# Performance work log

Hardware: AMD Instinct MI355X
Metric: run time of the kernel (lower is better)

The kernel has to match this reference:

```python
import jax, jax.numpy as jnp
import numpy as np

D_MODEL = 1024
N_HEADS = 16
D_Q = 64
D_V = 64
N_SEG = 16
EPS_LN = 1e-5
EPS_MEM = 1e-6


def setup_inputs() -> dict:
    key = jax.random.key(0)
    ks = jax.random.split(key, 10)
    N, T = 4, 4096
    inp = {
        "query_sequences": jax.random.normal(ks[0], (N, T, D_MODEL), dtype=jnp.float32),
        "key_sequences": jax.random.normal(ks[1], (N, T, D_MODEL), dtype=jnp.float32),
        "value_sequences": jax.random.normal(ks[2], (N, T, D_MODEL), dtype=jnp.float32),
        "Wq": jax.random.normal(ks[3], (D_MODEL, N_HEADS * D_Q), dtype=jnp.float32) * 0.02,
        "Wk": jax.random.normal(ks[4], (D_MODEL, N_HEADS * D_Q), dtype=jnp.float32) * 0.02,
        "Wv": jax.random.normal(ks[5], (D_MODEL, N_HEADS * D_V), dtype=jnp.float32) * 0.02,
        "Wo": jax.random.normal(ks[6], (N_HEADS * D_V, D_MODEL), dtype=jnp.float32) * 0.02,
        "ln_w": jnp.ones((D_MODEL,), dtype=jnp.float32),
        "ln_b": jnp.zeros((D_MODEL,), dtype=jnp.float32),
        "beta": jnp.ones((1,), dtype=jnp.float32),
    }
    return inp


def _layer_norm(x, w, b):
    mu = jnp.mean(x, axis=-1, keepdims=True)
    var = jnp.var(x, axis=-1, keepdims=True)
    return (x - mu) * jax.lax.rsqrt(var + EPS_LN) * w + b


def reference(query_sequences, key_sequences, value_sequences, Wq, Wk, Wv, Wo, ln_w, ln_b, beta):
    N, t, _ = query_sequences.shape
    S = t // N_SEG  # segment length (256)

    # qkv_norm applied to q, and (self-attention) to k and v as well
    qn = _layer_norm(query_sequences, ln_w, ln_b)
    kn = _layer_norm(key_sequences, ln_w, ln_b)
    vn = _layer_norm(value_sequences, ln_w, ln_b)

    # project and split heads -> [N, H, t, d]
    qh = (qn @ Wq).reshape(N, t, N_HEADS, D_Q).transpose(0, 2, 1, 3)
    kh = (kn @ Wk).reshape(N, t, N_HEADS, D_Q).transpose(0, 2, 1, 3)
    vh = (vn @ Wv).reshape(N, t, N_HEADS, D_V).transpose(0, 2, 1, 3)

    # segment: [N_SEG, N, H, S, d] so lax.scan iterates segments sequentially
    seg = lambda x, d: x.reshape(N, N_HEADS, N_SEG, S, d).transpose(2, 0, 1, 3, 4)
    q_segs, k_segs, v_segs = seg(qh, D_Q), seg(kh, D_Q), seg(vh, D_V)

    b_gate = jax.nn.sigmoid(beta)[0]            # scalar mixing gate
    scale = 1.0 / np.sqrt(D_Q).astype(np.float32)
    causal = jnp.tril(jnp.ones((S, S), dtype=bool))

    def step(carry, xs):
        mem, z = carry                          # [N,H,Dq,Dv], [N,H,Dq]
        qs, ks_, vs = xs                        # [N,H,S,d]
        sq = jax.nn.elu(qs) + 1.0
        sk = jax.nn.elu(ks_) + 1.0
        # retrieve from compressive memory
        num = jnp.einsum('nhsd,nhde->nhse', sq, mem)
        den = jnp.einsum('nhsd,nhd->nhs', sq, z)[..., None] + EPS_MEM
        a_mem = num / den                       # [N,H,S,Dv]
        # local causal softmax attention within the segment
        scores = jnp.einsum('nhsd,nhtd->nhst', qs, ks_) * scale
        scores = jnp.where(causal, scores, -jnp.inf)
        probs = jax.nn.softmax(scores, axis=-1)
        attn = jnp.einsum('nhst,nhtd->nhsd', probs, vs)
        out = b_gate * a_mem + (1.0 - b_gate) * attn
        # linear memory update
        mem = mem + jnp.einsum('nhsd,nhse->nhde', sk, vs)
        z = z + sk.sum(axis=2)
        return (mem, z), out

    mem0 = jnp.zeros((N, N_HEADS, D_Q, D_V), dtype=query_sequences.dtype)
    z0 = jnp.zeros((N, N_HEADS, D_Q), dtype=query_sequences.dtype)
    _, outs = jax.lax.scan(step, (mem0, z0), (q_segs, k_segs, v_segs))

    # outs: [N_SEG, N, H, S, Dv] -> [N, t, H*Dv]
    seqs = outs.transpose(1, 0, 3, 2, 4).reshape(N, t, N_HEADS * D_V)
    return seqs @ Wo
```

## Files before the change

kernel.cpp:

```cpp
#include <hip/hip_runtime.h>
#include <stdint.h>
#include <math.h>


typedef __attribute__((ext_vector_type(8))) short bf16x8_t;
typedef __attribute__((ext_vector_type(4))) short short4_t;
typedef __attribute__((ext_vector_type(4))) float f32x4;

__device__ __forceinline__ float bf2f(short s){
  union { unsigned u; float f; } v; v.u = ((unsigned)(unsigned short)s) << 16; return v.f;
}
__device__ __forceinline__ short f2bf(float f){
  union { float fl; unsigned u; } v; v.fl = f;
  unsigned r = v.u + 0x7FFFu + ((v.u >> 16) & 1u);
  return (short)(unsigned short)(r >> 16);
}
__device__ __forceinline__ f32x4 mfma16(bf16x8_t a, bf16x8_t b, f32x4 c){
  return __builtin_amdgcn_mfma_f32_16x16x32_bf16(a, b, c, 0, 0, 0);
}
__device__ __forceinline__ void gl_lds16(const short* g, short* l){
  __builtin_amdgcn_global_load_lds((const __attribute__((address_space(1))) void*)g,
                                   (__attribute__((address_space(3))) void*)l, 16, 0, 0);
}

__global__ __launch_bounds__(256) void ln_kernel(const float* __restrict__ x,
                                                 const float* __restrict__ gw,
                                                 const float* __restrict__ gb,
                                                 short* __restrict__ out){
  const int row = blockIdx.x, tid = threadIdx.x;
  const float4 v = *reinterpret_cast<const float4*>(x + (size_t)row*1024 + tid*4);
  float s  = v.x + v.y + v.z + v.w;
  float s2 = v.x*v.x + v.y*v.y + v.z*v.z + v.w*v.w;
  #pragma unroll
  for (int off = 1; off < 64; off <<= 1){
    s  += __shfl_xor(s,  off);
    s2 += __shfl_xor(s2, off);
  }
  __shared__ float red[8];
  if ((tid & 63) == 0){ red[tid>>6] = s; red[4 + (tid>>6)] = s2; }
  __syncthreads();
  s  = red[0] + red[1] + red[2] + red[3];
  s2 = red[4] + red[5] + red[6] + red[7];
  const float mu  = s * (1.0f/1024.0f);
  const float var = s2 * (1.0f/1024.0f) - mu*mu;
  const float rs  = rsqrtf(var + 1e-5f);
  const float4 wv = *reinterpret_cast<const float4*>(gw + tid*4);
  const float4 bv = *reinterpret_cast<const float4*>(gb + tid*4);
  short4_t o;
  o[0] = f2bf((v.x-mu)*rs*wv.x + bv.x);
  o[1] = f2bf((v.y-mu)*rs*wv.y + bv.y);
  o[2] = f2bf((v.z-mu)*rs*wv.z + bv.z);
  o[3] = f2bf((v.w-mu)*rs*wv.w + bv.w);
  *reinterpret_cast<short4_t*>(out + (size_t)row*1024 + tid*4) = o;
}

__global__ __launch_bounds__(256) void wcast(const float* __restrict__ W, short* __restrict__ Wt){
  __shared__ float tile[64][65];
  const int bx = blockIdx.x, by = blockIdx.y, tid = threadIdx.x;
  #pragma unroll
  for (int p=0;p<4;++p){
    int idx = p*256 + tid;
    int r = idx >> 4, c4 = (idx & 15) << 2;
    const float4 v = *reinterpret_cast<const float4*>(W + (size_t)(by*64 + r)*1024 + bx*64 + c4);
    tile[r][c4+0] = v.x; tile[r][c4+1] = v.y; tile[r][c4+2] = v.z; tile[r][c4+3] = v.w;
  }
  __syncthreads();
  #pragma unroll
  for (int p=0;p<4;++p){
    int idx = p*256 + tid;
    int r = idx >> 4, c4 = (idx & 15) << 2;
    short4_t o;
    o[0] = f2bf(tile[c4+0][r]); o[1] = f2bf(tile[c4+1][r]);
    o[2] = f2bf(tile[c4+2][r]); o[3] = f2bf(tile[c4+3][r]);
    *reinterpret_cast<short4_t*>(Wt + (size_t)(bx*64 + r)*1024 + by*64 + c4) = o;
  }
}

__global__ __launch_bounds__(512, 2) void gemm256(const short* __restrict__ A, const short* __restrict__ Bt,
                                                  void* __restrict__ C, int mode){
  extern __shared__ short smem[];
  short* As = smem;
  short* Bs = smem + 32768;
  const int tid = threadIdx.x;
  const int m0 = blockIdx.x * 256;
  const int c0 = blockIdx.y * 256;
  const int lane = tid & 63, wid = tid >> 6;
  const int wr = wid >> 2, wc = wid & 3;
  const int l15 = lane & 15, lhi = lane >> 4;

  const int r0 = tid >> 2,         s0 = tid & 3;
  const int r1 = (512 + tid) >> 2, s1 = tid & 3;
  const int g0 = s0 ^ (r0 & 3) ^ ((r0 >> 2) & 3);
  const int g1 = s1 ^ (r1 & 3) ^ ((r1 >> 2) & 3);
  const short* Ag0 = A  + (size_t)(m0 + r0)*1024 + g0*8;
  const short* Ag1 = A  + (size_t)(m0 + r1)*1024 + g1*8;
  const short* Bg0 = Bt + (size_t)(c0 + r0)*1024 + g0*8;
  const short* Bg1 = Bt + (size_t)(c0 + r1)*1024 + g1*8;

  f32x4 acc[8][4];
  #pragma unroll
  for (int m=0;m<8;++m)
    #pragma unroll
    for (int n=0;n<4;++n) acc[m][n] = (f32x4){0.f,0.f,0.f,0.f};

  #define STAGE_A(t) { int _b=((t)&3)<<13, _k=(t)<<5; \
      gl_lds16(Ag0+_k, &As[_b + tid*8]); gl_lds16(Ag1+_k, &As[_b + 4096 + tid*8]); }
  #define STAGE_B(t) { int _b=((t)&3)<<13, _k=(t)<<5; \
      gl_lds16(Bg0+_k, &Bs[_b + tid*8]); gl_lds16(Bg1+_k, &Bs[_b + 4096 + tid*8]); }

  STAGE_A(0); STAGE_B(0);
  STAGE_A(1); STAGE_B(1);
  STAGE_A(2); STAGE_B(2);
  asm volatile("s_waitcnt vmcnt(8)" ::: "memory");
  __builtin_amdgcn_s_barrier();

  for (int t = 0; t < 32; ++t){
    const short* Ab = &As[(t & 3) << 13];
    const short* Bb = &Bs[(t & 3) << 13];
    bf16x8_t bfrag[4], afrag[4];
    #pragma unroll
    for (int n=0;n<4;++n){
      int r = wc*64 + n*16 + l15;
      bfrag[n] = *reinterpret_cast<const bf16x8_t*>(&Bb[r*32 + ((lhi ^ (r & 3) ^ ((r >> 2) & 3)) << 3)]);
    }
    #pragma unroll
    for (int m=0;m<4;++m){
      int r = wr*128 + m*16 + l15;
      afrag[m] = *reinterpret_cast<const bf16x8_t*>(&Ab[r*32 + ((lhi ^ (r & 3) ^ ((r >> 2) & 3)) << 3)]);
    }
    if (t < 29) STAGE_A(t+3);
    __builtin_amdgcn_s_barrier();
    __builtin_amdgcn_s_setprio(1);
    #pragma unroll
    for (int m=0;m<4;++m)
      #pragma unroll
      for (int n=0;n<4;++n)
        acc[m][n] = mfma16(afrag[m], bfrag[n], acc[m][n]);
    __builtin_amdgcn_s_setprio(0);
    __builtin_amdgcn_s_barrier();
    #pragma unroll
    for (int m=0;m<4;++m){
      int r = wr*128 + 64 + m*16 + l15;
      afrag[m] = *reinterpret_cast<const bf16x8_t*>(&Ab[r*32 + ((lhi ^ (r & 3) ^ ((r >> 2) & 3)) << 3)]);
    }
    if (t < 29) STAGE_B(t+3);
    __builtin_amdgcn_s_barrier();
    __builtin_amdgcn_s_setprio(1);
    #pragma unroll
    for (int m=0;m<4;++m)
      #pragma unroll
      for (int n=0;n<4;++n)
        acc[4+m][n] = mfma16(afrag[m], bfrag[n], acc[4+m][n]);
    __builtin_amdgcn_s_setprio(0);
    if (t < 29)       { asm volatile("s_waitcnt vmcnt(8)" ::: "memory"); }
    else if (t == 29) { asm volatile("s_waitcnt vmcnt(4)" ::: "memory"); }
    else if (t == 30) { asm volatile("s_waitcnt vmcnt(0)" ::: "memory"); }
    __builtin_amdgcn_s_barrier();
  }
  #undef STAGE_A
  #undef STAGE_B

  if (mode == 0){
    short* Cb = (short*)C;
    #pragma unroll
    for (int m=0;m<8;++m)
      #pragma unroll
      for (int n=0;n<4;++n)
        #pragma unroll
        for (int j=0;j<4;++j){
          int row = m0 + wr*128 + m*16 + lhi*4 + j;
          int col = c0 + wc*64 + n*16 + l15;
          size_t oidx = ((size_t)((row>>12)*16 + (col>>6)) * 4096 + (size_t)(row & 4095)) * 64 + (col & 63);
          Cb[oidx] = f2bf(acc[m][n][j]);
        }
  } else if (mode == 2){
    short* Cb = (short*)C;
    #pragma unroll
    for (int m=0;m<8;++m)
      #pragma unroll
      for (int n=0;n<4;++n){
        int rowb = m0 + wr*128 + m*16 + lhi*4;
        int col  = c0 + wc*64 + n*16 + l15;
        int nh = ((rowb>>12)<<4) + (col>>6);
        int e  = col & 63;
        int tt = rowb & 4095;
        short4_t o;
        #pragma unroll
        for (int j=0;j<4;++j) o[j] = f2bf(acc[m][n][j]);
        *reinterpret_cast<short4_t*>(&Cb[((size_t)nh*64 + e)*4096 + tt]) = o;
      }
  } else {
    float* Cf = (float*)C;
    #pragma unroll
    for (int m=0;m<8;++m)
      #pragma unroll
      for (int n=0;n<4;++n)
        #pragma unroll
        for (int j=0;j<4;++j){
          int row = m0 + wr*128 + m*16 + lhi*4 + j;
          int col = c0 + wc*64 + n*16 + l15;
          Cf[(size_t)row*1024 + col] = acc[m][n][j];
        }
  }
}

__global__ __launch_bounds__(256) void stageA(const short* __restrict__ kh, const short* __restrict__ vhT,
                                              short* __restrict__ delta_b, float* __restrict__ zd){
  const int seg = blockIdx.x, nh = blockIdx.y, tid = threadIdx.x;
  const int lane = tid & 63, w = tid >> 6;
  const int l15 = lane & 15, lhi = lane >> 4;
  __shared__ short skT[64*256];
  const size_t thead = (size_t)nh*4096 + (size_t)seg*256;

  #pragma unroll
  for (int ch=0; ch<8; ++ch){
    int s  = ch*32 + (tid>>3);
    int lc = (tid&7)*8;
    bf16x8_t kv = *reinterpret_cast<const bf16x8_t*>(kh + (thead + s)*64 + lc);
    #pragma unroll
    for (int j=0;j<8;++j){
      float f = bf2f(kv[j]);
      short sv = f2bf((f > 0.f) ? (f + 1.f) : __expf(f));
      int d = lc + j;
      int bo = ((d*256 + s) << 1) ^ (((d>>3)&7) << 4);
      *reinterpret_cast<short*>(reinterpret_cast<char*>(skT) + bo) = sv;
    }
  }
  __syncthreads();

  bf16x8_t ones;
  #pragma unroll
  for (int i=0;i<8;++i) ones[i] = (short)0x3F80;

  f32x4 dacc[4], zacc[4];
  #pragma unroll
  for (int jf=0;jf<4;++jf){ dacc[jf] = (f32x4){0.f,0.f,0.f,0.f}; zacc[jf] = (f32x4){0.f,0.f,0.f,0.f}; }

  #pragma unroll
  for (int ks=0; ks<8; ++ks){
    bf16x8_t av = *reinterpret_cast<const bf16x8_t*>(
        vhT + ((size_t)nh*64 + w*16 + l15)*4096 + (size_t)seg*256 + ks*32 + lhi*8);
    #pragma unroll
    for (int jf=0;jf<4;++jf){
      int d  = jf*16 + l15;
      int so = ks*32 + lhi*8;
      int bo = ((d*256 + so) << 1) ^ (((d>>3)&7) << 4);
      bf16x8_t bk = *reinterpret_cast<const bf16x8_t*>(reinterpret_cast<char*>(skT) + bo);
      dacc[jf] = mfma16(av, bk, dacc[jf]);
      if (w == 0) zacc[jf] = mfma16(ones, bk, zacc[jf]);
    }
  }

  short* dp = delta_b + (size_t)(seg*64 + nh)*4096;
  #pragma unroll
  for (int jf=0;jf<4;++jf)
    #pragma unroll
    for (int j=0;j<4;++j)
      dp[(w*16 + lhi*4 + j)*64 + jf*16 + l15] = f2bf(dacc[jf][j]);
  if (w == 0 && lhi == 0){
    #pragma unroll
    for (int jf=0;jf<4;++jf)
      zd[(size_t)(seg*64 + nh)*64 + jf*16 + l15] = zacc[jf][0];
  }
}

__global__ __launch_bounds__(256) void stageB(const short* __restrict__ delta_b, const float* __restrict__ zd,
                                              short* __restrict__ mpre_b, float* __restrict__ zpre){
  const int c = blockIdx.x, nh = blockIdx.y, tid = threadIdx.x;
  const int idx = c*256 + tid;
  float acc = 0.f;
  for (int seg=0; seg<16; ++seg){
    size_t b = (size_t)(seg*64 + nh)*4096 + idx;
    mpre_b[b] = f2bf(acc);
    acc += bf2f(delta_b[b]);
  }
  if (c == 0 && tid < 64){
    float za = 0.f;
    for (int seg=0; seg<16; ++seg){
      size_t zb = (size_t)(seg*64 + nh)*64 + tid;
      zpre[zb] = za;
      za += zd[zb];
    }
  }
}

__global__ __launch_bounds__(256, 3) void stageC(const short* __restrict__ qh, const short* __restrict__ kh,
    const short* __restrict__ vhT, const short* __restrict__ mpre_b, const float* __restrict__ z_pre,
    const float* __restrict__ beta, short* __restrict__ seqs)
{
  const int half = blockIdx.x;
  const int seg  = blockIdx.y;
  const int nh   = blockIdx.z;
  const int tid = threadIdx.x;
  const int lane = tid & 63, w = tid >> 6;
  const int l15 = lane & 15, lhi = lane >> 4;

  __shared__ short mt[64][72];
  __shared__ float zl[64];
  __shared__ short pl[4][32][72];

  const size_t thead = (size_t)nh*4096 + (size_t)seg*256;

  {
    const short* mp = mpre_b + (size_t)(seg*64 + nh)*4096;
    bf16x8_t a0 = *reinterpret_cast<const bf16x8_t*>(mp + tid*16);
    bf16x8_t a1 = *reinterpret_cast<const bf16x8_t*>(mp + tid*16 + 8);
    int e = tid >> 2, d0 = (tid & 3) * 16;
    *reinterpret_cast<bf16x8_t*>(&mt[e][d0])     = a0;
    *reinterpret_cast<bf16x8_t*>(&mt[e][d0 + 8]) = a1;
    if (tid < 64) zl[tid] = z_pre[(size_t)(seg*64 + nh)*64 + tid];
  }
  __syncthreads();

  const float bg = 1.f / (1.f + __expf(-beta[0]));
  const float scale = 0.125f;
  bf16x8_t ones;
  #pragma unroll
  for (int i=0;i<8;++i) ones[i] = (short)0x3F80;

  const int tile = half ? (7 - w) : w;
  const int nkt  = (tile >> 1) + 1;
  const int rb   = tile * 32;

  bf16x8_t aq[2][2];
  #pragma unroll
  for (int m=0;m<2;++m)
    #pragma unroll
    for (int ks=0;ks<2;++ks)
      aq[m][ks] = *reinterpret_cast<const bf16x8_t*>(qh + (thead + rb + m*16 + l15)*64 + ks*32 + lhi*8);

  float m_run[2][4], l_run[2][4];
  f32x4 o_acc[2][4];
  #pragma unroll
  for (int m=0;m<2;++m){
    #pragma unroll
    for (int j=0;j<4;++j){ m_run[m][j] = -INFINITY; l_run[m][j] = 0.f; }
    #pragma unroll
    for (int jf=0;jf<4;++jf) o_acc[m][jf] = (f32x4){0.f,0.f,0.f,0.f};
  }

  for (int kt = 0; kt < nkt; ++kt){
    f32x4 s_acc[2][4];
    #pragma unroll
    for (int m=0;m<2;++m)
      #pragma unroll
      for (int jf=0;jf<4;++jf) s_acc[m][jf] = (f32x4){0.f,0.f,0.f,0.f};
    #pragma unroll
    for (int ks=0;ks<2;++ks){
      bf16x8_t bk[4];
      #pragma unroll
      for (int jf=0;jf<4;++jf)
        bk[jf] = *reinterpret_cast<const bf16x8_t*>(kh + (thead + kt*64 + jf*16 + l15)*64 + ks*32 + lhi*8);
      #pragma unroll
      for (int m=0;m<2;++m)
        #pragma unroll
        for (int jf=0;jf<4;++jf)
          s_acc[m][jf] = mfma16(aq[m][ks], bk[jf], s_acc[m][jf]);
    }
    float mnew[2][4];
    #pragma unroll
    for (int m=0;m<2;++m)
      #pragma unroll
      for (int j=0;j<4;++j) mnew[m][j] = m_run[m][j];
    const bool lastkt = (kt == nkt - 1);
    #pragma unroll
    for (int m=0;m<2;++m)
      #pragma unroll
      for (int jf=0;jf<4;++jf)
        #pragma unroll
        for (int j=0;j<4;++j){
          float vv = s_acc[m][jf][j] * scale;
          if (lastkt){
            int sr = rb + m*16 + lhi*4 + j;
            int tc = kt*64 + jf*16 + l15;
            if (tc > sr) vv = -INFINITY;
          }
          s_acc[m][jf][j] = vv;
          mnew[m][j] = fmaxf(mnew[m][j], vv);
        }
    #pragma unroll
    for (int m=0;m<2;++m)
      #pragma unroll
      for (int j=0;j<4;++j){
        #pragma unroll
        for (int off=1; off<16; off<<=1)
          mnew[m][j] = fmaxf(mnew[m][j], __shfl_xor(mnew[m][j], off));
        float corr = __expf(m_run[m][j] - mnew[m][j]);
        m_run[m][j] = mnew[m][j];
        l_run[m][j] *= corr;
        #pragma unroll
        for (int jf=0;jf<4;++jf) o_acc[m][jf][j] *= corr;
      }
    #pragma unroll
    for (int m=0;m<2;++m)
      #pragma unroll
      for (int jf=0;jf<4;++jf)
        #pragma unroll
        for (int j=0;j<4;++j){
          float pv = __expf(s_acc[m][jf][j] - mnew[m][j]);
          pl[w][m*16 + lhi*4 + j][jf*16 + l15] = f2bf(pv);
        }
    f32x4 ls[2];
    ls[0] = (f32x4){0.f,0.f,0.f,0.f};
    ls[1] = (f32x4){0.f,0.f,0.f,0.f};
    #pragma unroll
    for (int ks2=0;ks2<2;++ks2){
      bf16x8_t ap[2], bv[4];
      #pragma unroll
      for (int m=0;m<2;++m)
        ap[m] = *reinterpret_cast<const bf16x8_t*>(&pl[w][m*16 + l15][ks2*32 + lhi*8]);
      #pragma unroll
      for (int jf=0;jf<4;++jf)
        bv[jf] = *reinterpret_cast<const bf16x8_t*>(
            vhT + ((size_t)nh*64 + jf*16 + l15)*4096 + (size_t)seg*256 + kt*64 + ks2*32 + lhi*8);
      #pragma unroll
      for (int m=0;m<2;++m){
        ls[m] = mfma16(ap[m], ones, ls[m]);
        #pragma unroll
        for (int jf=0;jf<4;++jf)
          o_acc[m][jf] = mfma16(ap[m], bv[jf], o_acc[m][jf]);
      }
    }
    #pragma unroll
    for (int m=0;m<2;++m)
      #pragma unroll
      for (int j=0;j<4;++j) l_run[m][j] += ls[m][j];
  }

  bf16x8_t sq[2][2];
  #pragma unroll
  for (int m=0;m<2;++m)
    #pragma unroll
    for (int ks=0;ks<2;++ks)
      #pragma unroll
      for (int i=0;i<8;++i){
        float f = bf2f(aq[m][ks][i]);
        sq[m][ks][i] = f2bf((f > 0.f) ? (f + 1.f) : __expf(f));
      }
  bf16x8_t bz[2];
  #pragma unroll
  for (int ks=0;ks<2;++ks)
    #pragma unroll
    for (int i=0;i<8;++i) bz[ks][i] = f2bf(zl[ks*32 + lhi*8 + i]);

  f32x4 n_acc[2][4], d_acc[2];
  #pragma unroll
  for (int m=0;m<2;++m){
    d_acc[m] = (f32x4){0.f,0.f,0.f,0.f};
    #pragma unroll
    for (int jf=0;jf<4;++jf) n_acc[m][jf] = (f32x4){0.f,0.f,0.f,0.f};
  }
  #pragma unroll
  for (int ks=0;ks<2;++ks){
    bf16x8_t bm[4];
    #pragma unroll
    for (int jf=0;jf<4;++jf)
      bm[jf] = *reinterpret_cast<const bf16x8_t*>(&mt[jf*16 + l15][ks*32 + lhi*8]);
    #pragma unroll
    for (int m=0;m<2;++m){
      #pragma unroll
      for (int jf=0;jf<4;++jf) n_acc[m][jf] = mfma16(sq[m][ks], bm[jf], n_acc[m][jf]);
      d_acc[m] = mfma16(sq[m][ks], bz[ks], d_acc[m]);
    }
  }

  const int nb = nh >> 4, hh = nh & 15;
  #pragma unroll
  for (int m=0;m<2;++m)
    #pragma unroll
    for (int jf=0;jf<4;++jf)
      #pragma unroll
      for (int j=0;j<4;++j){
        float attn = o_acc[m][jf][j] / l_run[m][j];
        float amem = n_acc[m][jf][j] / (d_acc[m][j] + 1e-6f);
        float ov = bg*amem + (1.f-bg)*attn;
        int srow = rb + m*16 + lhi*4 + j;
        seqs[((size_t)nb*4096 + (size_t)seg*256 + srow)*1024 + hh*64 + jf*16 + l15] = f2bf(ov);
      }
}

extern "C" void kernel_launch(void* const* d_in, const int* in_sizes, int n_in,
                              void* d_out, int out_size, void* d_ws, size_t ws_size,
                              hipStream_t stream){
  (void)in_sizes; (void)n_in; (void)out_size; (void)ws_size;
  const float* q    = (const float*)d_in[0];
  const float* k    = (const float*)d_in[1];
  const float* v    = (const float*)d_in[2];
  const float* Wq   = (const float*)d_in[3];
  const float* Wk   = (const float*)d_in[4];
  const float* Wv   = (const float*)d_in[5];
  const float* Wo   = (const float*)d_in[6];
  const float* lnw  = (const float*)d_in[7];
  const float* lnb  = (const float*)d_in[8];
  const float* beta = (const float*)d_in[9];
  char* ws = (char*)d_ws;
  const size_t MB = 1024ull*1024ull;
  short* WqT    = (short*)(ws + 0*MB);
  short* WkT    = (short*)(ws + 2*MB);
  short* WvT    = (short*)(ws + 4*MB);
  short* WoT    = (short*)(ws + 6*MB);
  short* xn     = (short*)(ws + 8*MB);
  short* seqs   = xn;
  short* qh     = (short*)(ws + 40*MB);
  short* kh     = (short*)(ws + 72*MB);
  short* vhT    = (short*)(ws + 104*MB);
  short* delta_b= (short*)(ws + 136*MB);
  float* zd     = (float*)(ws + 144*MB);
  short* mpre_b = (short*)(ws + 145*MB);
  float* zpre   = (float*)(ws + 153*MB);

  dim3 tg(16,16);
  wcast<<<tg,256,0,stream>>>(Wq, WqT);
  wcast<<<tg,256,0,stream>>>(Wk, WkT);
  wcast<<<tg,256,0,stream>>>(Wv, WvT);
  wcast<<<tg,256,0,stream>>>(Wo, WoT);

  dim3 gg(64,4);
  const size_t lds_gemm = 131072;
  ln_kernel<<<16384,256,0,stream>>>(q, lnw, lnb, xn);
  gemm256<<<gg,512,lds_gemm,stream>>>(xn, WqT, (void*)qh, 0);
  ln_kernel<<<16384,256,0,stream>>>(k, lnw, lnb, xn);
  gemm256<<<gg,512,lds_gemm,stream>>>(xn, WkT, (void*)kh, 0);
  ln_kernel<<<16384,256,0,stream>>>(v, lnw, lnb, xn);
  gemm256<<<gg,512,lds_gemm,stream>>>(xn, WvT, (void*)vhT, 2);

  stageA<<<dim3(16,64),256,0,stream>>>(kh, vhT, delta_b, zd);
  stageB<<<dim3(16,64),256,0,stream>>>(delta_b, zd, mpre_b, zpre);
  stageC<<<dim3(2,16,64),256,0,stream>>>(qh, kh, vhT, mpre_b, zpre, beta, seqs);
  gemm256<<<gg,512,lds_gemm,stream>>>(seqs, WoT, d_out, 1);
}
```

Before: 342.9 us.

## Use K=64 double-buffered GEMM stages and read memory state directly from global

```diff
diff --git a/kernel.cpp b/kernel.cpp
--- a/kernel.cpp
+++ b/kernel.cpp
@@ -88,14 +88,14 @@
   const int wr = wid >> 2, wc = wid & 3;
   const int l15 = lane & 15, lhi = lane >> 4;
 
-  const int r0 = tid >> 2,         s0 = tid & 3;
-  const int r1 = (512 + tid) >> 2, s1 = tid & 3;
-  const int g0 = s0 ^ (r0 & 3) ^ ((r0 >> 2) & 3);
-  const int g1 = s1 ^ (r1 & 3) ^ ((r1 >> 2) & 3);
-  const short* Ag0 = A  + (size_t)(m0 + r0)*1024 + g0*8;
-  const short* Ag1 = A  + (size_t)(m0 + r1)*1024 + g1*8;
-  const short* Bg0 = Bt + (size_t)(c0 + r0)*1024 + g0*8;
-  const short* Bg1 = Bt + (size_t)(c0 + r1)*1024 + g1*8;
+  const short* Asrc[4]; const short* Bsrc[4];
+  #pragma unroll
+  for (int p=0;p<4;++p){
+    int i = tid + 512*p;
+    int r = i >> 3, g = (i & 7) ^ (r & 7);
+    Asrc[p] = A  + (size_t)(m0 + r)*1024 + g*8;
+    Bsrc[p] = Bt + (size_t)(c0 + r)*1024 + g*8;
+  }
 
   f32x4 acc[8][4];
   #pragma unroll
@@ -103,58 +103,96 @@
     #pragma unroll
     for (int n=0;n<4;++n) acc[m][n] = (f32x4){0.f,0.f,0.f,0.f};
 
-  #define STAGE_A(t) { int _b=((t)&3)<<13, _k=(t)<<5; \
-      gl_lds16(Ag0+_k, &As[_b + tid*8]); gl_lds16(Ag1+_k, &As[_b + 4096 + tid*8]); }
-  #define STAGE_B(t) { int _b=((t)&3)<<13, _k=(t)<<5; \
-      gl_lds16(Bg0+_k, &Bs[_b + tid*8]); gl_lds16(Bg1+_k, &Bs[_b + 4096 + tid*8]); }
+  #define STAGE_A(t) { short* _d=&As[((t)&1)<<14]; int _k=(t)<<6; \
+      gl_lds16(Asrc[0]+_k, _d+tid*8); gl_lds16(Asrc[1]+_k, _d+4096+tid*8); \
+      gl_lds16(Asrc[2]+_k, _d+8192+tid*8); gl_lds16(Asrc[3]+_k, _d+12288+tid*8); }
+  #define STAGE_B(t) { short* _d=&Bs[((t)&1)<<14]; int _k=(t)<<6; \
+      gl_lds16(Bsrc[0]+_k, _d+tid*8); gl_lds16(Bsrc[1]+_k, _d+4096+tid*8); \
+      gl_lds16(Bsrc[2]+_k, _d+8192+tid*8); gl_lds16(Bsrc[3]+_k, _d+12288+tid*8); }
 
   STAGE_A(0); STAGE_B(0);
-  STAGE_A(1); STAGE_B(1);
-  STAGE_A(2); STAGE_B(2);
-  asm volatile("s_waitcnt vmcnt(8)" ::: "memory");
+  asm volatile("s_waitcnt vmcnt(0)" ::: "memory");
   __builtin_amdgcn_s_barrier();
 
-  for (int t = 0; t < 32; ++t){
-    const short* Ab = &As[(t & 3) << 13];
-    const short* Bb = &Bs[(t & 3) << 13];
-    bf16x8_t bfrag[4], afrag[4];
-    #pragma unroll
-    for (int n=0;n<4;++n){
-      int r = wc*64 + n*16 + l15;
-      bfrag[n] = *reinterpret_cast<const bf16x8_t*>(&Bb[r*32 + ((lhi ^ (r & 3) ^ ((r >> 2) & 3)) << 3)]);
-    }
+  for (int t = 0; t < 16; ++t){
+    const short* Ab = &As[(t & 1) << 14];
+    const short* Bb = &Bs[(t & 1) << 14];
+    bf16x8_t af[4][2], bfr[4][2];
     #pragma unroll
     for (int m=0;m<4;++m){
       int r = wr*128 + m*16 + l15;
-      afrag[m] = *reinterpret_cast<const bf16x8_t*>(&Ab[r*32 + ((lhi ^ (r & 3) ^ ((r >> 2) & 3)) << 3)]);
-    }
-    if (t < 29) STAGE_A(t+3);
-    __builtin_amdgcn_s_barrier();
+      #pragma unroll
+      for (int ks=0;ks<2;++ks){
+        int sl = (ks*4 + lhi) ^ (r & 7);
+        af[m][ks] = *reinterpret_cast<const bf16x8_t*>(&Ab[r*64 + sl*8]);
+      }
+    }
+    #pragma unroll
+    for (int n=0;n<2;++n){
+      int r = wc*64 + n*16 + l15;
+      #pragma unroll
+      for (int ks=0;ks<2;++ks){
+        int sl = (ks*4 + lhi) ^ (r & 7);
+        bfr[n][ks] = *reinterpret_cast<const bf16x8_t*>(&Bb[r*64 + sl*8]);
+      }
+    }
+    if (t < 15) STAGE_A(t+1);
     __builtin_amdgcn_s_setprio(1);
     #pragma unroll
     for (int m=0;m<4;++m)
       #pragma unroll
-      for (int n=0;n<4;++n)
-        acc[m][n] = mfma16(afrag[m], bfrag[n], acc[m][n]);
+      for (int n=0;n<2;++n)
+        #pragma unroll
+        for (int ks=0;ks<2;++ks)
+          acc[m][n] = mfma16(af[m][ks], bfr[n][ks], acc[m][n]);
     __builtin_amdgcn_s_setprio(0);
-    __builtin_amdgcn_s_barrier();
+    #pragma unroll
+    for (int n=2;n<4;++n){
+      int r = wc*64 + n*16 + l15;
+      #pragma unroll
+      for (int ks=0;ks<2;++ks){
+        int sl = (ks*4 + lhi) ^ (r & 7);
+        bfr[n][ks] = *reinterpret_cast<const bf16x8_t*>(&Bb[r*64 + sl*8]);
+      }
+    }
+    if (t < 15) STAGE_B(t+1);
+    __builtin_amdgcn_s_setprio(1);
+    #pragma unroll
+    for (int m=0;m<4;++m)
+      #pragma unroll
+      for (int n=2;n<4;++n)
+        #pragma unroll
+        for (int ks=0;ks<2;++ks)
+          acc[m][n] = mfma16(af[m][ks], bfr[n][ks], acc[m][n]);
+    __builtin_amdgcn_s_setprio(0);
     #pragma unroll
     for (int m=0;m<4;++m){
       int r = wr*128 + 64 + m*16 + l15;
-      afrag[m] = *reinterpret_cast<const bf16x8_t*>(&Ab[r*32 + ((lhi ^ (r & 3) ^ ((r >> 2) & 3)) << 3)]);
-    }
-    if (t < 29) STAGE_B(t+3);
-    __builtin_amdgcn_s_barrier();
+      #pragma unroll
+      for (int ks=0;ks<2;++ks){
+        int sl = (ks*4 + lhi) ^ (r & 7);
+        af[m][ks] = *reinterpret_cast<const bf16x8_t*>(&Ab[r*64 + sl*8]);
+      }
+    }
     __builtin_amdgcn_s_setprio(1);
     #pragma unroll
     for (int m=0;m<4;++m)
       #pragma unroll
-      for (int n=0;n<4;++n)
-        acc[4+m][n] = mfma16(afrag[m], bfrag[n], acc[4+m][n]);
+      for (int n=0;n<2;++n)
+        #pragma unroll
+        for (int ks=0;ks<2;++ks)
+          acc[4+m][n] = mfma16(af[m][ks], bfr[n][ks], acc[4+m][n]);
     __builtin_amdgcn_s_setprio(0);
-    if (t < 29)       { asm volatile("s_waitcnt vmcnt(8)" ::: "memory"); }
-    else if (t == 29) { asm volatile("s_waitcnt vmcnt(4)" ::: "memory"); }
-    else if (t == 30) { asm volatile("s_waitcnt vmcnt(0)" ::: "memory"); }
+    __builtin_amdgcn_s_setprio(1);
+    #pragma unroll
+    for (int m=0;m<4;++m)
+      #pragma unroll
+      for (int n=2;n<4;++n)
+        #pragma unroll
+        for (int ks=0;ks<2;++ks)
+          acc[4+m][n] = mfma16(af[m][ks], bfr[n][ks], acc[4+m][n]);
+    __builtin_amdgcn_s_setprio(0);
+    asm volatile("s_waitcnt vmcnt(0)" ::: "memory");
     __builtin_amdgcn_s_barrier();
   }
   #undef STAGE_A
@@ -295,21 +333,12 @@
   const int lane = tid & 63, w = tid >> 6;
   const int l15 = lane & 15, lhi = lane >> 4;
 
-  __shared__ short mt[64][72];
   __shared__ float zl[64];
   __shared__ short pl[4][32][72];
 
   const size_t thead = (size_t)nh*4096 + (size_t)seg*256;
 
-  {
-    const short* mp = mpre_b + (size_t)(seg*64 + nh)*4096;
-    bf16x8_t a0 = *reinterpret_cast<const bf16x8_t*>(mp + tid*16);
-    bf16x8_t a1 = *reinterpret_cast<const bf16x8_t*>(mp + tid*16 + 8);
-    int e = tid >> 2, d0 = (tid & 3) * 16;
-    *reinterpret_cast<bf16x8_t*>(&mt[e][d0])     = a0;
-    *reinterpret_cast<bf16x8_t*>(&mt[e][d0 + 8]) = a1;
-    if (tid < 64) zl[tid] = z_pre[(size_t)(seg*64 + nh)*64 + tid];
-  }
+  if (tid < 64) zl[tid] = z_pre[(size_t)(seg*64 + nh)*64 + tid];
   __syncthreads();
 
   const float bg = 1.f / (1.f + __expf(-beta[0]));
@@ -443,6 +472,7 @@
     #pragma unroll
     for (int i=0;i<8;++i) bz[ks][i] = f2bf(zl[ks*32 + lhi*8 + i]);
 
+  const short* mpbase = mpre_b + (size_t)(seg*64 + nh)*4096;
   f32x4 n_acc[2][4], d_acc[2];
   #pragma unroll
   for (int m=0;m<2;++m){
@@ -455,7 +485,7 @@
     bf16x8_t bm[4];
     #pragma unroll
     for (int jf=0;jf<4;++jf)
-      bm[jf] = *reinterpret_cast<const bf16x8_t*>(&mt[jf*16 + l15][ks*32 + lhi*8]);
+      bm[jf] = *reinterpret_cast<const bf16x8_t*>(mpbase + (jf*16 + l15)*64 + ks*32 + lhi*8);
     #pragma unroll
     for (int m=0;m<2;++m){
       #pragma unroll
```

Result: faster. 328.5 us (-4.2%).
